# Performance work log

Hardware: AMD Instinct MI355X
Metric: run time of the kernel (lower is better)

## Reference

```python
import jax, jax.numpy as jnp
import numpy as np

N_EMBD = 512
N_EXPERTS = 4
TOP_K = 2
D_FF = 4 * N_EMBD


def setup_inputs() -> dict:
    key = jax.random.key(0)
    k_x, k_g, k_w1, k_w2 = jax.random.split(key, 4)
    b, t = 8, 2048
    x = jax.random.normal(k_x, (b, t, N_EMBD), dtype=jnp.float32)
    # Linear layers are bias-free; kaiming-uniform-ish init scale
    gate_w = jax.random.normal(k_g, (N_EMBD, N_EXPERTS), dtype=jnp.float32) * (1.0 / np.sqrt(N_EMBD))
    w1 = jax.random.normal(k_w1, (N_EXPERTS, N_EMBD, D_FF), dtype=jnp.float32) * (1.0 / np.sqrt(N_EMBD))
    w2 = jax.random.normal(k_w2, (N_EXPERTS, D_FF, N_EMBD), dtype=jnp.float32) * (1.0 / np.sqrt(D_FF))
    return {"x": x, "gate_w": gate_w, "w1": w1, "w2": w2}


def reference(x, gate_w, w1, w2):
    # Eval mode: UnitCenteredNoise and Dropout are identity.
    b, t, c = x.shape
    xf = x.reshape(b * t, c)                         # [N, C]
    n = xf.shape[0]

    gate_logits = xf @ gate_w                        # [N, E]
    gate_probs = jax.nn.softmax(gate_logits, axis=-1)
    top_w, top_i = jax.lax.top_k(gate_probs, TOP_K)  # [N, K]
    top_w = top_w / jnp.clip(jnp.sum(top_w, axis=-1, keepdims=True), 1e-6)

    # Sparse router weights [N, E]: zeros except normalized top-k probs.
    router_sparse = jnp.zeros((n, N_EXPERTS), dtype=top_w.dtype)
    router_sparse = router_sparse.at[jnp.arange(n)[:, None], top_i].set(top_w)

    # Per-expert MLP on all tokens, combined with the sparse router weights.
    # Mathematically identical to the masked dispatch/combine in the original.
    h = jnp.einsum('nc,ech->enh', xf, w1)            # [E, N, 4C]
    h = jax.nn.gelu(h, approximate=False)            # torch F.gelu default = erf
    y = jnp.einsum('enh,ehc->enc', h, w2)            # [E, N, C]
    out_flat = jnp.einsum('ne,enc->nc', router_sparse, y)

    return out_flat.reshape(b, t, c), router_sparse
```

## Files before the change

### kernel.cpp

```cpp
#include <hip/hip_runtime.h>
#include <hip/hip_fp16.h>


#define NTOK  16384
#define CDIM  512
#define FF    2048
#define NEXP  4
#define CAP   33280
#define NBLK  260
#define BM    128
#define BN1   128
#define BN2   64
#define BK    64
#define CPAD  32

typedef _Float16 f16;
typedef __attribute__((ext_vector_type(8))) _Float16 f16x8;
typedef __attribute__((ext_vector_type(4))) _Float16 f16x4;
typedef __attribute__((ext_vector_type(4))) float f32x4;

__device__ __forceinline__ void gload16(const void* g, void* l) {
  __builtin_amdgcn_global_load_lds(
      (const __attribute__((address_space(1))) unsigned int*)g,
      (__attribute__((address_space(3))) unsigned int*)l, 16, 0, 0);
}

__device__ __forceinline__ float gelu_fast(float v) {
  float az = fabsf(v) * 0.7071067811865476f;
  float t = __builtin_amdgcn_rcpf(fmaf(0.3275911f, az, 1.0f));
  float p = fmaf(fmaf(fmaf(fmaf(1.061405429f, t, -1.453152027f), t,
                           1.421413741f), t, -0.284496736f), t, 0.254829592f) * t;
  float e = __builtin_amdgcn_exp2f(az * az * -1.4426950408889634f);
  float erfa = fmaf(-p, e, 1.0f);
  float u = copysignf(erfa, v);
  return 0.5f * v * (1.0f + u);
}

__device__ __forceinline__ int xcd_swz(int bid, int nwg) {
  return (bid & 7) * (nwg >> 3) + (bid >> 3);
}


__global__ __launch_bounds__(256) void k_init(int* list, int* cnt) {
  int i = blockIdx.x * 256 + threadIdx.x;
  if (i < CAP) list[i] = -1;
  if (i < 4) cnt[i * CPAD] = 0;
}

__global__ __launch_bounds__(256) void k_cast_t(const float* __restrict__ in,
                                                f16* __restrict__ out, int R, int Cc) {
  __shared__ f16 T[64][72];
  int ez = blockIdx.z;
  const float* ine = in + (size_t)ez * R * Cc;
  f16* oute = out + (size_t)ez * R * Cc;
  int c0 = blockIdx.x * 64;
  int r0 = blockIdx.y * 64;
  int t = threadIdx.x;
  {
    int rr = t >> 2, cc = (t & 3) * 16;
    const float* src = ine + (size_t)(r0 + rr) * Cc + c0 + cc;
    union { f16 h[16]; uint4 u[2]; } pk;
#pragma unroll
    for (int j = 0; j < 16; j += 4) {
      float4 a = *(const float4*)(src + j);
      pk.h[j] = (f16)a.x; pk.h[j + 1] = (f16)a.y;
      pk.h[j + 2] = (f16)a.z; pk.h[j + 3] = (f16)a.w;
    }
    *(uint4*)&T[rr][cc] = pk.u[0];
    *(uint4*)&T[rr][cc + 8] = pk.u[1];
  }
  __syncthreads();
  {
    int oc = t >> 2, orr = (t & 3) * 16;
    union { f16 h[16]; uint4 u[2]; } pk;
#pragma unroll
    for (int j = 0; j < 16; ++j) pk.h[j] = T[orr + j][oc];
    f16* dst = oute + (size_t)(c0 + oc) * R + r0 + orr;
    *(uint4*)dst = pk.u[0];
    *(uint4*)(dst + 8) = pk.u[1];
  }
}


__global__ __launch_bounds__(256) void k_router(const float* __restrict__ x,
                                                const float* __restrict__ gw,
                                                f16* __restrict__ xh,
                                                float* __restrict__ rout,
                                                float4* __restrict__ tokinfo,
                                                int* __restrict__ cnt) {
  __shared__ int lcnt[4];
  int tid = threadIdx.x;
  if (tid < 4) lcnt[tid] = 0;
  __syncthreads();
  int wv = tid >> 6, lane = tid & 63;
  const float4* g = ((const float4*)gw) + lane * 8;
  float4 gv[8];
#pragma unroll
  for (int j = 0; j < 8; ++j) gv[j] = g[j];

  int tok0 = blockIdx.x * 64 + wv * 16;
  for (int i = 0; i < 16; ++i) {
    int tok = tok0 + i;
    const float4* xr = (const float4*)(x + (size_t)tok * CDIM + lane * 8);
    float4 a0 = xr[0], a1 = xr[1];
    union { f16 h[8]; uint4 u; } pk;
    pk.h[0] = (f16)a0.x; pk.h[1] = (f16)a0.y; pk.h[2] = (f16)a0.z; pk.h[3] = (f16)a0.w;
    pk.h[4] = (f16)a1.x; pk.h[5] = (f16)a1.y; pk.h[6] = (f16)a1.z; pk.h[7] = (f16)a1.w;
    *(uint4*)(xh + (size_t)tok * CDIM + lane * 8) = pk.u;
    float xv[8] = {a0.x, a0.y, a0.z, a0.w, a1.x, a1.y, a1.z, a1.w};
    float l0 = 0, l1 = 0, l2 = 0, l3 = 0;
#pragma unroll
    for (int j = 0; j < 8; ++j) {
      float4 g4 = gv[j];
      l0 = fmaf(xv[j], g4.x, l0); l1 = fmaf(xv[j], g4.y, l1);
      l2 = fmaf(xv[j], g4.z, l2); l3 = fmaf(xv[j], g4.w, l3);
    }
#pragma unroll
    for (int off = 32; off; off >>= 1) {
      l0 += __shfl_xor(l0, off); l1 += __shfl_xor(l1, off);
      l2 += __shfl_xor(l2, off); l3 += __shfl_xor(l3, off);
    }
    if (lane == 0) {
      float lg[4] = {l0, l1, l2, l3};
      float m = fmaxf(fmaxf(lg[0], lg[1]), fmaxf(lg[2], lg[3]));
      float p[4], s = 0.f;
#pragma unroll
      for (int e = 0; e < 4; ++e) { p[e] = expf(lg[e] - m); s += p[e]; }
      int i0 = 0;
#pragma unroll
      for (int e = 1; e < 4; ++e) if (lg[e] > lg[i0]) i0 = e;
      int i1 = -1;
#pragma unroll
      for (int e = 0; e < 4; ++e)
        if (e != i0 && (i1 < 0 || lg[e] > lg[i1])) i1 = e;
      float p0 = p[i0] / s, p1 = p[i1] / s;
      float ss = fmaxf(p0 + p1, 1e-6f);
      float w0 = p0 / ss, w1v = p1 / ss;
      float r[4] = {0.f, 0.f, 0.f, 0.f};
      r[i0] = w0; r[i1] = w1v;
      *(float4*)(rout + tok * 4) = make_float4(r[0], r[1], r[2], r[3]);
      float4 ti;
      ti.x = __int_as_float(i0); ti.y = __int_as_float(i1); ti.z = w0; ti.w = w1v;
      tokinfo[tok] = ti;
      atomicAdd(&lcnt[i0], 1);
      atomicAdd(&lcnt[i1], 1);
    }
  }
  __syncthreads();
  if (tid < 4) atomicAdd(cnt + tid * CPAD, lcnt[tid]);
}

__global__ void k_bases(const int* __restrict__ cnt, int* __restrict__ base,
                        int* __restrict__ cursor) {
  if (threadIdx.x == 0 && blockIdx.x == 0) {
    int b = 0;
#pragma unroll
    for (int e = 0; e < 4; ++e) {
      base[e] = b; cursor[e * CPAD] = b;
      b += (cnt[e * CPAD] + 127) & ~127;
    }
    base[4] = b;
  }
}

__global__ __launch_bounds__(256) void k_assign(const float4* __restrict__ tokinfo,
                                                int* cursor, int* __restrict__ list,
                                                int2* __restrict__ tokslot) {
  __shared__ int lcnt[4], lbase[4];
  int tid = threadIdx.x;
  if (tid < 4) lcnt[tid] = 0;
  __syncthreads();
  int t0 = blockIdx.x * 1024 + tid * 4;
  float4 ti[4]; int lo0[4], lo1[4];
#pragma unroll
  for (int j = 0; j < 4; ++j) {
    ti[j] = tokinfo[t0 + j];
    lo0[j] = atomicAdd(&lcnt[__float_as_int(ti[j].x)], 1);
    lo1[j] = atomicAdd(&lcnt[__float_as_int(ti[j].y)], 1);
  }
  __syncthreads();
  if (tid < 4) lbase[tid] = atomicAdd(cursor + tid * CPAD, lcnt[tid]);
  __syncthreads();
#pragma unroll
  for (int j = 0; j < 4; ++j) {
    int s0 = lbase[__float_as_int(ti[j].x)] + lo0[j];
    list[s0] = t0 + j;
    int s1 = lbase[__float_as_int(ti[j].y)] + lo1[j];
    list[s1] = t0 + j;
    tokslot[t0 + j] = make_int2(s0, s1);
  }
}


__global__ __launch_bounds__(256) void k_gemm1(const f16* __restrict__ xh,
                                               const f16* __restrict__ w1t,
                                               const int* __restrict__ list,
                                               const int* __restrict__ base,
                                               f16* __restrict__ H, int cb, int nwg) {
  __shared__ __align__(16) char smem[65536 + 512];
  int* slist = (int*)(smem + 65536);
  int tid = threadIdx.x;
  int wk = xcd_swz(blockIdx.x, nwg);
  int bx = wk >> 4, by = wk & 15;
  int m0 = (cb + bx) * BM;
  int mloc = bx * BM;
  int h0 = by * BN1;
  int e = 0;
#pragma unroll
  for (int i = 1; i < 4; ++i) if (m0 >= base[i]) e = i;
  if (tid < BM) {
    int v = list[m0 + tid];
    slist[tid] = v < 0 ? 0 : v;
  }
  __syncthreads();

  int tokr[4];
#pragma unroll
  for (int i = 0; i < 4; ++i) tokr[i] = slist[i * 32 + (tid >> 3)];

  const f16* wB = w1t + (size_t)(e * FF + h0) * CDIM;
  int kbs = ((tid & 7) * 16) ^ (((tid >> 3) & 7) << 4);

  f32x4 acc[4][4] = {};
  int lane = tid & 63, w = tid >> 6, wr = w >> 1, wc = w & 1;

  auto stage = [&](int kk, int p) {
    char* s = smem + p * 32768;
#pragma unroll
    for (int i = 0; i < 4; ++i) {
      gload16(xh + (size_t)tokr[i] * CDIM + kk * BK + (kbs >> 1),
              s + i * 4096 + tid * 16);
    }
#pragma unroll
    for (int i = 0; i < 4; ++i) {
      int row = i * 32 + (tid >> 3);
      gload16(wB + (size_t)row * CDIM + kk * BK + (kbs >> 1),
              s + 16384 + i * 4096 + tid * 16);
    }
  };

  auto compute = [&](int p) {
    const char* s = smem + p * 32768;
#pragma unroll
    for (int ks = 0; ks < 2; ++ks) {
      f16x8 af[4], bfr[4];
      int kb = ks * 64 + (lane >> 4) * 16;
#pragma unroll
      for (int fr = 0; fr < 4; ++fr) {
        int row = wr * 64 + fr * 16 + (lane & 15);
        af[fr] = *(const f16x8*)(s + row * 128 + (kb ^ ((row & 7) << 4)));
      }
#pragma unroll
      for (int fc = 0; fc < 4; ++fc) {
        int col = wc * 64 + fc * 16 + (lane & 15);
        bfr[fc] = *(const f16x8*)(s + 16384 + col * 128 + (kb ^ ((col & 7) << 4)));
      }
#pragma unroll
      for (int fr = 0; fr < 4; ++fr)
#pragma unroll
        for (int fc = 0; fc < 4; ++fc)
          acc[fr][fc] = __builtin_amdgcn_mfma_f32_16x16x32_f16(af[fr], bfr[fc],
                                                               acc[fr][fc], 0, 0, 0);
    }
  };

  stage(0, 0);
  __syncthreads();
  for (int kk = 0; kk < 8; ++kk) {
    if (kk < 7) stage(kk + 1, (kk + 1) & 1);
    __builtin_amdgcn_sched_barrier(0);
    __builtin_amdgcn_s_setprio(1);
    compute(kk & 1);
    __builtin_amdgcn_s_setprio(0);
    __syncthreads();
  }

#pragma unroll
  for (int fr = 0; fr < 4; ++fr)
#pragma unroll
    for (int fc = 0; fc < 4; ++fc)
#pragma unroll
      for (int i = 0; i < 4; ++i) {
        int row = wr * 64 + fr * 16 + (lane >> 4) * 4 + i;
        int col = wc * 64 + fc * 16 + (lane & 15);
        float v = gelu_fast(acc[fr][fc][i]);
        int off = (row * 256 + col * 2) ^ ((row & 7) << 4);
        *(f16*)(smem + off) = (f16)v;
      }
  __syncthreads();
#pragma unroll
  for (int j = 0; j < 8; ++j) {
    int row = j * 16 + (tid >> 4);
    int colb = ((tid & 15) * 16) ^ ((row & 7) << 4);
    uint4 v = *(const uint4*)(smem + row * 256 + colb);
    *(uint4*)((char*)H + ((size_t)(mloc + row) * FF + h0) * 2 + (tid & 15) * 16) = v;
  }
}


__global__ __launch_bounds__(256) void k_gemm2(const f16* __restrict__ H,
                                               const f16* __restrict__ w2t,
                                               const int* __restrict__ base,
                                               f16* __restrict__ Y, int cb, int nwg) {
  __shared__ __align__(16) char smem[49152];
  int tid = threadIdx.x;
  int wk = xcd_swz(blockIdx.x, nwg);
  int bx = wk >> 3, by = wk & 7;
  int m0 = (cb + bx) * BM;
  int mloc = bx * BM;
  int c0 = by * BN2;
  int e = 0;
#pragma unroll
  for (int i = 1; i < 4; ++i) if (m0 >= base[i]) e = i;

  const f16* pA = H + (size_t)mloc * FF;
  const f16* wB = w2t + (size_t)(e * CDIM + c0) * FF;
  int kbs = ((tid & 7) * 16) ^ (((tid >> 3) & 7) << 4);

  f32x4 acc[4][2] = {};
  int lane = tid & 63, w = tid >> 6, wr = w >> 1, wc = w & 1;

  auto stage = [&](int kk, int p) {
    char* s = smem + p * 24576;
#pragma unroll
    for (int i = 0; i < 4; ++i) {
      int row = i * 32 + (tid >> 3);
      gload16(pA + (size_t)row * FF + kk * BK + (kbs >> 1),
              s + i * 4096 + tid * 16);
    }
#pragma unroll
    for (int i = 0; i < 2; ++i) {
      int row = i * 32 + (tid >> 3);
      gload16(wB + (size_t)row * FF + kk * BK + (kbs >> 1),
              s + 16384 + i * 4096 + tid * 16);
    }
  };

  auto compute = [&](int p) {
    const char* s = smem + p * 24576;
#pragma unroll
    for (int ks = 0; ks < 2; ++ks) {
      f16x8 af[4], bfr[2];
      int kb = ks * 64 + (lane >> 4) * 16;
#pragma unroll
      for (int fr = 0; fr < 4; ++fr) {
        int row = wr * 64 + fr * 16 + (lane & 15);
        af[fr] = *(const f16x8*)(s + row * 128 + (kb ^ ((row & 7) << 4)));
      }
#pragma unroll
      for (int fc = 0; fc < 2; ++fc) {
        int col = wc * 32 + fc * 16 + (lane & 15);
        bfr[fc] = *(const f16x8*)(s + 16384 + col * 128 + (kb ^ ((col & 7) << 4)));
      }
#pragma unroll
      for (int fr = 0; fr < 4; ++fr)
#pragma unroll
        for (int fc = 0; fc < 2; ++fc)
          acc[fr][fc] = __builtin_amdgcn_mfma_f32_16x16x32_f16(af[fr], bfr[fc],
                                                               acc[fr][fc], 0, 0, 0);
    }
  };

  stage(0, 0);
  __syncthreads();
  for (int kk = 0; kk < 32; ++kk) {
    if (kk < 31) stage(kk + 1, (kk + 1) & 1);
    __builtin_amdgcn_sched_barrier(0);
    __builtin_amdgcn_s_setprio(1);
    compute(kk & 1);
    __builtin_amdgcn_s_setprio(0);
    __syncthreads();
  }

#pragma unroll
  for (int fr = 0; fr < 4; ++fr)
#pragma unroll
    for (int fc = 0; fc < 2; ++fc)
#pragma unroll
      for (int i = 0; i < 4; ++i) {
        int row = wr * 64 + fr * 16 + (lane >> 4) * 4 + i;
        int col = wc * 32 + fc * 16 + (lane & 15);
        int off = (row * 128 + col * 2) ^ ((row & 7) << 4);
        *(f16*)(smem + off) = (f16)acc[fr][fc][i];
      }
  __syncthreads();
#pragma unroll
  for (int j = 0; j < 4; ++j) {
    int row = j * 32 + (tid >> 3);
    int colb = ((tid & 7) * 16) ^ ((row & 7) << 4);
    uint4 v = *(const uint4*)(smem + row * 128 + colb);
    *(uint4*)((char*)Y + ((size_t)(m0 + row) * CDIM + c0) * 2 + (tid & 7) * 16) = v;
  }
}


__global__ __launch_bounds__(256) void k_combine(const f16* __restrict__ Y,
                                                 const float4* __restrict__ tokinfo,
                                                 const int2* __restrict__ tokslot,
                                                 float* __restrict__ out) {
  int gid = blockIdx.x * 256 + threadIdx.x;
  int tok = gid >> 7;
  int cc = (gid & 127) * 4;
  int2 sl = tokslot[tok];
  float4 ti = tokinfo[tok];
  f16x4 y0 = *(const f16x4*)(Y + (size_t)sl.x * CDIM + cc);
  f16x4 y1 = *(const f16x4*)(Y + (size_t)sl.y * CDIM + cc);
  float w0 = ti.z, w1 = ti.w;
  float4 o;
  o.x = w0 * (float)y0[0] + w1 * (float)y1[0];
  o.y = w0 * (float)y0[1] + w1 * (float)y1[1];
  o.z = w0 * (float)y0[2] + w1 * (float)y1[2];
  o.w = w0 * (float)y0[3] + w1 * (float)y1[3];
  *(float4*)(out + (size_t)tok * CDIM + cc) = o;
}


extern "C" void kernel_launch(void* const* d_in, const int* in_sizes, int n_in,
                              void* d_out, int out_size, void* d_ws, size_t ws_size,
                              hipStream_t stream) {
  const float* x  = (const float*)d_in[0];
  const float* gw = (const float*)d_in[1];
  const float* w1 = (const float*)d_in[2];
  const float* w2 = (const float*)d_in[3];
  float* out  = (float*)d_out;
  float* rout = out + (size_t)NTOK * CDIM;

  char* ws = (char*)d_ws;
  f16* xh      = (f16*)ws;      ws += (size_t)NTOK * CDIM * 2;
  f16* w1t     = (f16*)ws;      ws += (size_t)NEXP * FF * CDIM * 2;
  f16* w2t     = (f16*)ws;      ws += (size_t)NEXP * FF * CDIM * 2;
  f16* Ybuf    = (f16*)ws;      ws += (size_t)CAP * CDIM * 2;
  float4* tokinfo = (float4*)ws; ws += (size_t)NTOK * 16;
  int2* tokslot = (int2*)ws;    ws += (size_t)NTOK * 8;
  int* list    = (int*)ws;      ws += (size_t)CAP * 4;
  int* cnt     = (int*)ws;      ws += 4 * CPAD * 4;
  int* base    = (int*)ws;      ws += 64;
  int* cursor  = (int*)ws;      ws += 4 * CPAD * 4;
  f16* Hbuf    = (f16*)ws;

  size_t base_bytes = (size_t)(ws - (char*)d_ws);
  const int opts[12] = {260, 130, 65, 52, 26, 20, 13, 10, 5, 4, 2, 1};
  int CB = 1;
  for (int oi = 0; oi < 12; ++oi) {
    if (base_bytes + (size_t)opts[oi] * BM * FF * 2 <= ws_size) { CB = opts[oi]; break; }
  }

  k_init<<<(CAP + 255) / 256, 256, 0, stream>>>(list, cnt);
  k_cast_t<<<dim3(FF / 64, CDIM / 64, NEXP), 256, 0, stream>>>(w1, w1t, CDIM, FF);
  k_cast_t<<<dim3(CDIM / 64, FF / 64, NEXP), 256, 0, stream>>>(w2, w2t, FF, CDIM);
  k_router<<<NTOK / 64, 256, 0, stream>>>(x, gw, xh, rout, tokinfo, cnt);
  k_bases<<<1, 64, 0, stream>>>(cnt, base, cursor);
  k_assign<<<NTOK / 1024, 256, 0, stream>>>(tokinfo, cursor, list, tokslot);

  for (int cb = 0; cb < NBLK; cb += CB) {
    int n1 = CB * 16, n2 = CB * 8;
    k_gemm1<<<n1, 256, 0, stream>>>(xh, w1t, list, base, Hbuf, cb, n1);
    k_gemm2<<<n2, 256, 0, stream>>>(Hbuf, w2t, base, Ybuf, cb, n2);
  }
  k_combine<<<NTOK * CDIM / 4 / 256, 256, 0, stream>>>(Ybuf, tokinfo, tokslot, out);
}
```

Baseline: 305.7 us.

## Deepen GEMM pipelines with vmcnt-based waits and triple buffering in GEMM2

GEMM1's loop now waits on vmcnt with raw barriers instead of a full __syncthreads, so the next stage's global-to-LDS loads stay in flight while the current tile is computed. GEMM2 moves from two to three LDS buffers (shared memory grows to 72KB) so loads run two stages ahead. The host also caps the chunk size at 65 blocks, so the two GEMMs launch in more, smaller chunks, which keeps the H buffer smaller and may help L2 reuse. The larger LDS use may lower occupancy, and the hand-written vmcnt counts depend on how many loads each stage issues.

```diff
diff --git a/kernel.cpp b/kernel.cpp
--- a/kernel.cpp
+++ b/kernel.cpp
@@ -265,15 +265,20 @@
   };
 
   stage(0, 0);
-  __syncthreads();
-  for (int kk = 0; kk < 8; ++kk) {
-    if (kk < 7) stage(kk + 1, (kk + 1) & 1);
+  for (int kk = 0; kk < 7; ++kk) {
+    stage(kk + 1, (kk + 1) & 1);
+    asm volatile("s_waitcnt vmcnt(8)" ::: "memory");
+    __builtin_amdgcn_s_barrier();
     __builtin_amdgcn_sched_barrier(0);
     __builtin_amdgcn_s_setprio(1);
     compute(kk & 1);
     __builtin_amdgcn_s_setprio(0);
-    __syncthreads();
-  }
+    __builtin_amdgcn_sched_barrier(0);
+    __builtin_amdgcn_s_barrier();
+  }
+  asm volatile("s_waitcnt vmcnt(0)" ::: "memory");
+  __builtin_amdgcn_s_barrier();
+  compute(1);
 
 #pragma unroll
   for (int fr = 0; fr < 4; ++fr)
@@ -302,7 +307,7 @@
                                                const f16* __restrict__ w2t,
                                                const int* __restrict__ base,
                                                f16* __restrict__ Y, int cb, int nwg) {
-  __shared__ __align__(16) char smem[49152];
+  __shared__ __align__(16) char smem[73728];
   int tid = threadIdx.x;
   int wk = xcd_swz(blockIdx.x, nwg);
   int bx = wk >> 3, by = wk & 7;
@@ -362,15 +367,25 @@
   };
 
   stage(0, 0);
-  __syncthreads();
-  for (int kk = 0; kk < 32; ++kk) {
-    if (kk < 31) stage(kk + 1, (kk + 1) & 1);
+  stage(1, 1);
+  for (int kk = 0; kk < 30; ++kk) {
+    stage(kk + 2, (kk + 2) % 3);
+    asm volatile("s_waitcnt vmcnt(12)" ::: "memory");
+    __builtin_amdgcn_s_barrier();
     __builtin_amdgcn_sched_barrier(0);
     __builtin_amdgcn_s_setprio(1);
-    compute(kk & 1);
+    compute(kk % 3);
     __builtin_amdgcn_s_setprio(0);
-    __syncthreads();
-  }
+    __builtin_amdgcn_sched_barrier(0);
+    __builtin_amdgcn_s_barrier();
+  }
+  asm volatile("s_waitcnt vmcnt(6)" ::: "memory");
+  __builtin_amdgcn_s_barrier();
+  compute(0);
+  __builtin_amdgcn_s_barrier();
+  asm volatile("s_waitcnt vmcnt(0)" ::: "memory");
+  __builtin_amdgcn_s_barrier();
+  compute(1);
 
 #pragma unroll
   for (int fr = 0; fr < 4; ++fr)
@@ -439,9 +454,9 @@
   f16* Hbuf    = (f16*)ws;
 
   size_t base_bytes = (size_t)(ws - (char*)d_ws);
-  const int opts[12] = {260, 130, 65, 52, 26, 20, 13, 10, 5, 4, 2, 1};
+  const int opts[10] = {65, 52, 26, 20, 13, 10, 5, 4, 2, 1};
   int CB = 1;
-  for (int oi = 0; oi < 12; ++oi) {
+  for (int oi = 0; oi < 10; ++oi) {
     if (base_bytes + (size_t)opts[oi] * BM * FF * 2 <= ws_size) { CB = opts[oi]; break; }
   }
 
```

Measured after the change: 374.9 us. +22.7%, slower.
